# Performance work log

Measured on AMD Instinct MI355X. Metric: run time of the kernel, lower is better.

## Reference

```python
import jax, jax.numpy as jnp
import numpy as np

B, CIN, CNECK, COUT = 8, 128, 128, 256
NV, NF = 10242, 20480  # icosphere level 5: nv = 10*4^5+2, nf = 20*4^5
EPS = 1e-5


def spmatmul(x, rows, cols, vals, m):
    # x: [..., N]; out[..., r] += vals[k] * x[..., cols[k]] for rows[k] == r
    g = x[..., cols] * vals
    return jnp.zeros(x.shape[:-1] + (m,), x.dtype).at[..., rows].add(g)


def conv1x1(x, w, b):
    # x: [B, Cin, N], w: [Cout, Cin], b: [Cout]
    return jnp.einsum('oi,bin->bon', w, x) + b[None, :, None]


def batchnorm1d(x, gamma, beta):
    # training-mode BN over (batch, spatial) per channel, biased variance
    mean = jnp.mean(x, axis=(0, 2), keepdims=True)
    var = jnp.var(x, axis=(0, 2), keepdims=True)
    xhat = (x - mean) * jax.lax.rsqrt(var + EPS)
    return gamma[None, :, None] * xhat + beta[None, :, None]


def setup_inputs() -> dict:
    key = jax.random.key(0)
    ks = jax.random.split(key, 16)

    def coo(k, nrows, per_row, ncols, scale):
        rows = jnp.repeat(jnp.arange(nrows, dtype=jnp.int32), per_row)
        cols = jax.random.randint(k, (nrows * per_row,), 0, ncols, dtype=jnp.int32)
        vals = jax.random.normal(jax.random.fold_in(k, 1), (nrows * per_row,), jnp.float32) * scale
        return rows, cols, vals

    Gr, Gc, Gv = coo(ks[0], 3 * NF, 3, NV, 0.5)
    Lr, Lc, Lv = coo(ks[1], NV, 7, NV, 0.3)
    Fr, Fc, Fv = coo(ks[2], NV, 6, NF, 1.0 / 6.0)

    def nrm(k, shape, scale=1.0):
        return jax.random.normal(k, shape, jnp.float32) * scale

    s_in = 1.0 / np.sqrt(CIN)
    s_nk = 1.0 / np.sqrt(CNECK)
    s_cf = 1.0 / np.sqrt(4 * CNECK)
    return {
        'x': nrm(ks[3], (B, CIN, NV)),
        'w1a': nrm(ks[4], (CNECK, CIN), s_in), 'b1a': nrm(ks[5], (CNECK,), s_in),
        'g1a': jnp.ones((CNECK,), jnp.float32), 'be1a': jnp.zeros((CNECK,), jnp.float32),
        'coeffs': nrm(ks[6], (CNECK * 4, CNECK), s_cf),
        'g2a': jnp.ones((CNECK,), jnp.float32), 'be2a': jnp.zeros((CNECK,), jnp.float32),
        'w3a': nrm(ks[7], (COUT, CNECK), s_nk), 'b3a': nrm(ks[8], (COUT,), s_nk),
        'g3a': jnp.ones((COUT,), jnp.float32), 'be3a': jnp.zeros((COUT,), jnp.float32),
        'w1b': nrm(ks[9], (COUT, CIN), s_in), 'b1b': nrm(ks[10], (COUT,), s_in),
        'g1b': jnp.ones((COUT,), jnp.float32), 'be1b': jnp.zeros((COUT,), jnp.float32),
        'G_vals': Gv, 'L_vals': Lv, 'F2V_vals': Fv,
        'EW': nrm(ks[11], (NF, 3)), 'NS': nrm(ks[12], (NF, 3)),
        'G_rows': Gr, 'G_cols': Gc,
        'L_rows': Lr, 'L_cols': Lc,
        'F2V_rows': Fr, 'F2V_cols': Fc,
    }


def mesh_conv(h, coeffs, G_rows, G_cols, G_vals, L_rows, L_cols, L_vals,
              F2V_rows, F2V_cols, F2V_vals, EW, NS):
    b, c, nv = h.shape
    # gradient on faces: [B,C,3*NF] -> [B,C,3,NF] -> [B,C,NF,3]
    grad_face = spmatmul(h, G_rows, G_cols, G_vals, 3 * NF)
    grad_face = grad_face.reshape(b, c, 3, NF).transpose(0, 1, 3, 2)
    laplacian = spmatmul(h, L_rows, L_cols, L_vals, NV)
    identity = h  # stride=1 => nv_prev == nv
    gf_ew = jnp.sum(grad_face * EW, axis=-1)  # [B,C,NF]
    gf_ns = jnp.sum(grad_face * NS, axis=-1)
    gv_ew = spmatmul(gf_ew, F2V_rows, F2V_cols, F2V_vals, NV)
    gv_ns = spmatmul(gf_ns, F2V_rows, F2V_cols, F2V_vals, NV)
    feat = jnp.stack([identity, laplacian, gv_ew, gv_ns], axis=-1)  # [B,C,NV,4]
    # [B,NV,C*4] @ [C*4,Cout] -> [B,Cout,NV]  (note: no bias added in original forward)
    out = jnp.matmul(feat.transpose(0, 2, 1, 3).reshape(b, nv, c * 4), coeffs)
    return out.transpose(0, 2, 1)


def reference(x, w1a, b1a, g1a, be1a, coeffs, g2a, be2a, w3a, b3a, g3a, be3a,
              w1b, b1b, g1b, be1b, G_vals, L_vals, F2V_vals, EW, NS,
              G_rows, G_cols, L_rows, L_cols, F2V_rows, F2V_cols):
    # shortcut branch: conv_1b -> bn_1b
    x2 = batchnorm1d(conv1x1(x, w1b, b1b), g1b, be1b)
    # main branch
    h = jax.nn.relu(batchnorm1d(conv1x1(x, w1a, b1a), g1a, be1a))
    h = mesh_conv(h, coeffs, G_rows, G_cols, G_vals, L_rows, L_cols, L_vals,
                  F2V_rows, F2V_cols, F2V_vals, EW, NS)
    h = jax.nn.relu(batchnorm1d(h, g2a, be2a))
    x1 = batchnorm1d(conv1x1(h, w3a, b3a), g3a, be3a)
    return jax.nn.relu(x1 + x2)
```

## Files before the change

### kernel.cpp

```cpp
#include <hip/hip_runtime.h>
#include <math.h>

#define BB   8
#define NVV  10242
#define NFF  20480
#define EPSBN 1e-5f
#define GRAM_BLOCKS 1288
#define RSPLIT 16
#define RCHUNK ((GRAM_BLOCKS + RSPLIT - 1) / RSPLIT)

typedef __attribute__((ext_vector_type(8))) short bf16x8_t;
typedef __attribute__((ext_vector_type(4))) float f32x4_t;

__device__ inline float bf2f(ushort u) {
    union { uint i; float f; } v; v.i = ((uint)u) << 16; return v.f;
}
__device__ inline ushort f2bf(float f) {
    union { float f; uint i; } v; v.f = f;
    const uint r = v.i + 0x7fffu + ((v.i >> 16) & 1u);
    return (ushort)(r >> 16);
}
__device__ inline void unpack2(uint w, float& lo, float& hi) {
    union { uint i; float f; } a, b;
    a.i = w << 16; b.i = w & 0xffff0000u;
    lo = a.f; hi = b.f;
}
__device__ inline uint pack2(float lo, float hi) {
    return (uint)f2bf(lo) | ((uint)f2bf(hi) << 16);
}
__device__ inline void fma8(const uint4 hv, const float w, float s[8]) {
    float lo, hi;
    unpack2(hv.x, lo, hi); s[0] = fmaf(w, lo, s[0]); s[1] = fmaf(w, hi, s[1]);
    unpack2(hv.y, lo, hi); s[2] = fmaf(w, lo, s[2]); s[3] = fmaf(w, hi, s[3]);
    unpack2(hv.z, lo, hi); s[4] = fmaf(w, lo, s[4]); s[5] = fmaf(w, hi, s[5]);
    unpack2(hv.w, lo, hi); s[6] = fmaf(w, lo, s[6]); s[7] = fmaf(w, hi, s[7]);
}
__device__ inline void fma8x2(const uint4 hv, const float wa, const float wb,
                              float sa[8], float sb[8]) {
    float lo, hi;
    unpack2(hv.x, lo, hi);
    sa[0] = fmaf(wa, lo, sa[0]); sb[0] = fmaf(wb, lo, sb[0]);
    sa[1] = fmaf(wa, hi, sa[1]); sb[1] = fmaf(wb, hi, sb[1]);
    unpack2(hv.y, lo, hi);
    sa[2] = fmaf(wa, lo, sa[2]); sb[2] = fmaf(wb, lo, sb[2]);
    sa[3] = fmaf(wa, hi, sa[3]); sb[3] = fmaf(wb, hi, sb[3]);
    unpack2(hv.z, lo, hi);
    sa[4] = fmaf(wa, lo, sa[4]); sb[4] = fmaf(wb, lo, sb[4]);
    sa[5] = fmaf(wa, hi, sa[5]); sb[5] = fmaf(wb, hi, sb[5]);
    unpack2(hv.w, lo, hi);
    sa[6] = fmaf(wa, lo, sa[6]); sb[6] = fmaf(wb, lo, sb[6]);
    sa[7] = fmaf(wa, hi, sa[7]); sb[7] = fmaf(wb, hi, sb[7]);
}
__device__ inline uint4 pack8(const float s[8]) {
    uint4 p;
    p.x = pack2(s[0], s[1]); p.y = pack2(s[2], s[3]);
    p.z = pack2(s[4], s[5]); p.w = pack2(s[6], s[7]);
    return p;
}

__global__ __launch_bounds__(256)
void gram_kernel(const float* __restrict__ x, float* __restrict__ gramPart,
                 float* __restrict__ xsumPart, uint* __restrict__ xTu)
{
    __shared__ __align__(16) ushort Ahi[128 * 64];
    __shared__ __align__(16) ushort Alo[128 * 64];
    const int t = threadIdx.x;
    const int l = t & 63, wid = t >> 6;
    const int l15 = l & 15, l4 = l >> 4;
    f32x4_t acc[2][8];
#pragma unroll
    for (int m = 0; m < 2; ++m)
#pragma unroll
        for (int n = 0; n < 8; ++n) acc[m][n] = (f32x4_t){0.f, 0.f, 0.f, 0.f};
    float xs[8] = {0.f, 0.f, 0.f, 0.f, 0.f, 0.f, 0.f, 0.f};

    const int cc = blockIdx.x;
    const int b = cc / 161, tb = cc % 161, v0 = tb * 64;
#pragma unroll
    for (int i = 0; i < 8; ++i) {
        const int item = t + (i << 8);
        const int c = item >> 4, vq = item & 15;
        const int gv = v0 + (vq << 2);
        const float* xp = x + ((size_t)b * 128 + c) * NVV + gv;
        float4 xv = make_float4(0.f, 0.f, 0.f, 0.f);
        if (gv + 4 <= NVV) {
            xv = *reinterpret_cast<const float4*>(xp);
        } else {
            if (gv     < NVV) xv.x = xp[0];
            if (gv + 1 < NVV) xv.y = xp[1];
        }
        xs[i] += xv.x + xv.y + xv.z + xv.w;
        const ushort h0 = f2bf(xv.x), h1 = f2bf(xv.y), h2 = f2bf(xv.z), h3 = f2bf(xv.w);
        const ushort e0 = f2bf(xv.x - bf2f(h0)), e1 = f2bf(xv.y - bf2f(h1));
        const ushort e2 = f2bf(xv.z - bf2f(h2)), e3 = f2bf(xv.w - bf2f(h3));
        uint2 hp, lp;
        hp.x = (uint)h0 | ((uint)h1 << 16); hp.y = (uint)h2 | ((uint)h3 << 16);
        lp.x = (uint)e0 | ((uint)e1 << 16); lp.y = (uint)e2 | ((uint)e3 << 16);
        const int byte = (c << 7) + (vq << 3);
        const int swz = byte ^ ((c & 7) << 4);
        *reinterpret_cast<uint2*>((char*)Ahi + swz) = hp;
        *reinterpret_cast<uint2*>((char*)Alo + swz) = lp;
    }
    __syncthreads();
    {
        const int v = t & 63, cq = t >> 6;
        const int gv = v0 + v;
        if (gv < NVV) {
            uint4* rowp = reinterpret_cast<uint4*>(xTu + ((size_t)b * NVV + gv) * 64) + (cq << 2);
#pragma unroll
            for (int k2 = 0; k2 < 4; ++k2) {
                uint wrd[4];
#pragma unroll
                for (int w2 = 0; w2 < 4; ++w2) {
                    const int c0 = (cq << 5) + (k2 << 3) + (w2 << 1);
                    const int b0 = ((c0) << 7) + (v << 1);
                    const int b1 = ((c0 + 1) << 7) + (v << 1);
                    const ushort q0 = *reinterpret_cast<const ushort*>((const char*)Ahi + (b0 ^ ((c0 & 7) << 4)));
                    const ushort q1 = *reinterpret_cast<const ushort*>((const char*)Ahi + (b1 ^ (((c0 + 1) & 7) << 4)));
                    wrd[w2] = (uint)q0 | ((uint)q1 << 16);
                }
                rowp[k2] = make_uint4(wrd[0], wrd[1], wrd[2], wrd[3]);
            }
        }
    }
#pragma unroll
    for (int kk2 = 0; kk2 < 2; ++kk2) {
        bf16x8_t ah[2], al[2];
#pragma unroll
        for (int m = 0; m < 2; ++m) {
            const int row = wid * 32 + m * 16 + l15;
            const int byte = (row << 7) + (kk2 << 6) + (l4 << 4);
            ah[m] = *reinterpret_cast<const bf16x8_t*>((const char*)Ahi + (byte ^ ((row & 7) << 4)));
            al[m] = *reinterpret_cast<const bf16x8_t*>((const char*)Alo + (byte ^ ((row & 7) << 4)));
        }
#pragma unroll
        for (int n = 0; n < 8; ++n) {
            const int rn = n * 16 + l15;
            const int byte = (rn << 7) + (kk2 << 6) + (l4 << 4);
            const bf16x8_t bh = *reinterpret_cast<const bf16x8_t*>((const char*)Ahi + (byte ^ ((rn & 7) << 4)));
            const bf16x8_t bl = *reinterpret_cast<const bf16x8_t*>((const char*)Alo + (byte ^ ((rn & 7) << 4)));
#pragma unroll
            for (int m = 0; m < 2; ++m) {
                acc[m][n] = __builtin_amdgcn_mfma_f32_16x16x32_bf16(ah[m], bh, acc[m][n], 0, 0, 0);
                acc[m][n] = __builtin_amdgcn_mfma_f32_16x16x32_bf16(ah[m], bl, acc[m][n], 0, 0, 0);
                acc[m][n] = __builtin_amdgcn_mfma_f32_16x16x32_bf16(al[m], bh, acc[m][n], 0, 0, 0);
            }
        }
    }
    float* gp = gramPart + (size_t)blockIdx.x * 16384;
#pragma unroll
    for (int m = 0; m < 2; ++m)
#pragma unroll
        for (int n = 0; n < 8; ++n)
#pragma unroll
            for (int j = 0; j < 4; ++j) {
                const int row = wid * 32 + m * 16 + l4 * 4 + j;
                const int col = n * 16 + l15;
                gp[row * 128 + col] = acc[m][n][j];
            }
#pragma unroll
    for (int i = 0; i < 8; ++i) {
        xs[i] += __shfl_xor(xs[i], 1);
        xs[i] += __shfl_xor(xs[i], 2);
        xs[i] += __shfl_xor(xs[i], 4);
        xs[i] += __shfl_xor(xs[i], 8);
    }
    if ((l & 15) == 0) {
#pragma unroll
        for (int i = 0; i < 8; ++i)
            xsumPart[(size_t)blockIdx.x * 128 + wid * 4 + l4 + i * 16] = xs[i];
    }
}

__global__ __launch_bounds__(256)
void reduce_gram1_kernel(const float* __restrict__ gp, float* __restrict__ part2)
{
    const int e = blockIdx.x * 256 + threadIdx.x;
    const int y = blockIdx.y;
    const int i0 = y * RCHUNK;
    const int i1 = (i0 + RCHUNK < GRAM_BLOCKS) ? (i0 + RCHUNK) : GRAM_BLOCKS;
    float s = 0.f;
    for (int i = i0; i < i1; ++i) s += gp[(size_t)i * 16384 + e];
    part2[(size_t)y * 16384 + e] = s;
}

__global__ __launch_bounds__(256)
void reduce_gram2_kernel(const float* __restrict__ part2, const float* __restrict__ xp,
                         float* __restrict__ Gram, float* __restrict__ xsum)
{
    const int e = blockIdx.x * 256 + threadIdx.x;
    float s = 0.f;
#pragma unroll
    for (int y = 0; y < RSPLIT; ++y) s += part2[(size_t)y * 16384 + e];
    Gram[e] = s;
    if (blockIdx.x == 0 && threadIdx.x < 128) {
        float sx = 0.f;
        for (int i = 0; i < GRAM_BLOCKS; ++i) sx += xp[(size_t)i * 128 + threadIdx.x];
        xsum[threadIdx.x] = sx;
    }
}

__global__ __launch_bounds__(128)
void stats_ab_kernel(const float* __restrict__ Gram, const float* __restrict__ xsum,
                     const float* __restrict__ w1a, const float* __restrict__ g1a,
                     const float* __restrict__ be1a,
                     const float* __restrict__ w1b, const float* __restrict__ g1b,
                     const float* __restrict__ be1b,
                     float* __restrict__ alpha_a, float* __restrict__ beta_a,
                     float* __restrict__ alpha_b, float* __restrict__ beta_b)
{
    const int t = threadIdx.x;
    const int cc = blockIdx.x;
    const float invN = 1.f / (float)(BB * NVV);
    const bool isA = cc < 128;
    const int c = isA ? cc : cc - 128;
    const float* Wrow = isA ? (w1a + (size_t)c * 128) : (w1b + (size_t)c * 128);
    __shared__ float Wr[128];
    __shared__ float red[4];
    Wr[t] = Wrow[t];
    __syncthreads();
    float gi = 0.f;
    const float* Grow = Gram + (size_t)t * 128;
    for (int j = 0; j < 128; ++j) gi = fmaf(Grow[j], Wr[j], gi);
    float pi = Wr[t] * gi * invN;
    float qi = (xsum[t] * invN) * Wr[t];
    for (int off = 32; off > 0; off >>= 1) {
        pi += __shfl_down(pi, off);
        qi += __shfl_down(qi, off);
    }
    const int wid = t >> 6;
    if ((t & 63) == 0) { red[wid] = pi; red[2 + wid] = qi; }
    __syncthreads();
    if (t == 0) {
        const float P = red[0] + red[1], Q = red[2] + red[3];
        const float var = P - Q * Q;
        const float g = isA ? g1a[c] : g1b[c];
        const float be = isA ? be1a[c] : be1b[c];
        const float a = g * rsqrtf(var + EPSBN);
        if (isA) { alpha_a[c] = a; beta_a[c] = be - a * Q; }
        else     { alpha_b[c] = a; beta_b[c] = be - a * Q; }
    }
}

__global__ __launch_bounds__(256)
void prepack_weights_kernel(const float* __restrict__ w1a, const float* __restrict__ w1b,
                            const float* __restrict__ w3a, uint* __restrict__ wpk)
{
    const int j = blockIdx.x * 256 + threadIdx.x;
    const int seg = j >> 12;
    const int slab = seg >> 1, kc = (seg & 1) << 6;
    const int u = j & 4095;
    const int o = u >> 5;
    const int inner = (u << 2) & 127;
    const int inner0 = inner ^ ((o & 7) << 4);
    const int kp = inner0 >> 2;
    const float* W;
    if (slab == 0)      W = w1a;
    else if (slab <= 2) W = w1b + (size_t)(slab - 1) * 128 * 128;
    else                W = w3a + (size_t)(slab - 3) * 128 * 128;
    const float2 wv = *reinterpret_cast<const float2*>(&W[(size_t)o * 128 + kc + 2 * kp]);
    wpk[j] = pack2(wv.x, wv.y);
}

__global__ __launch_bounds__(256)
void prepack_coeffs_kernel(const float* __restrict__ coeffs, uint* __restrict__ cpk)
{
    const int j = blockIdx.x * 256 + threadIdx.x;
    const int chunk = j >> 12, u = j & 4095;
    const int o = u >> 5;
    const int inner = (u << 2) & 127;
    const int inner0 = inner ^ ((o & 7) << 4);
    const int p = inner0 >> 2;
    float v0f, v1f;
    if (chunk < 4) {
        const int q = chunk >> 1, c0 = (chunk & 1) << 6;
        const int row0 = (c0 + 2 * p) * 4 + q;
        v0f = coeffs[(size_t)row0 * 128 + o];
        v1f = coeffs[(size_t)(row0 + 4) * 128 + o];
    } else if (chunk < 6) {
        const int c0 = (chunk - 4) << 6;
        v0f = (o == c0 + 2 * p) ? 1.f : 0.f;
        v1f = (o == c0 + 2 * p + 1) ? 1.f : 0.f;
    } else {
        const int kc = chunk - 6;
        const int kg0 = kc * 64 + 2 * p;
        const int row0 = (kg0 < 128) ? (kg0 * 4 + 2) : ((kg0 - 128) * 4 + 3);
        const int row1 = (kg0 + 1 < 128) ? ((kg0 + 1) * 4 + 2) : ((kg0 + 1 - 128) * 4 + 3);
        v0f = coeffs[(size_t)row0 * 128 + o];
        v1f = coeffs[(size_t)row1 * 128 + o];
    }
    cpk[j] = pack2(v0f, v1f);
}

__global__ __launch_bounds__(256)
void build_meta_kernel(const float* __restrict__ Gv, const int* __restrict__ Gc,
                       const float* __restrict__ EW, const float* __restrict__ NSm,
                       int* __restrict__ colp, float2* __restrict__ wp)
{
    const int i = blockIdx.x * 256 + threadIdx.x;
    if (i >= NFF * 9) return;
    const int f = i / 9, m = i - f * 9;
    const int e = m / 3, jj = m - e * 3;
    const size_t gidx = ((size_t)e * NFF + f) * 3 + jj;
    const float g = Gv[gidx];
    colp[i] = Gc[gidx];
    wp[i] = make_float2(EW[f * 3 + e] * g, NSm[f * 3 + e] * g);
}

template <int MODE>
__global__ __launch_bounds__(256)
void mfma_conv_kernel(const ushort* __restrict__ Asrc, const uint4* __restrict__ wpk,
                      const float* __restrict__ aIn, const float* __restrict__ bIn,
                      const float* __restrict__ aA, const float* __restrict__ bA,
                      const float* __restrict__ aB, const float* __restrict__ bB,
                      ushort* __restrict__ hOut, ushort* __restrict__ x2Out,
                      ushort* __restrict__ x1Out,
                      float* __restrict__ statSum, float* __restrict__ statSsq)
{
    __shared__ __align__(16) ushort As[64 * 128];
    __shared__ __align__(16) ushort Bs[128 * 64];
    float* statS = (float*)Bs;
    float* statQ = (float*)Bs + 512;
    const int t = threadIdx.x;
    const int bid = blockIdx.x;
    const int b = bid & 7, vblk = bid >> 3;
    const int v0 = vblk * 64;
    const int l = t & 63, wid = t >> 6;
    const int l15 = l & 15, l4 = l >> 4;

#pragma unroll
    for (int i = 0; i < 4; ++i) {
        const int item = t + (i << 8);
        const int r = item >> 4, piece = item & 15;
        const int cb = piece * 8;
        const int v = v0 + r;
        uint4 pk = make_uint4(0u, 0u, 0u, 0u);
        if (v < NVV) {
            pk = *reinterpret_cast<const uint4*>(Asrc + ((size_t)b * NVV + v) * 128 + cb);
            if (MODE == 1) {
                float s[8];
                unpack2(pk.x, s[0], s[1]); unpack2(pk.y, s[2], s[3]);
                unpack2(pk.z, s[4], s[5]); unpack2(pk.w, s[6], s[7]);
                const float4 a0 = *reinterpret_cast<const float4*>(&aIn[cb]);
                const float4 a1 = *reinterpret_cast<const float4*>(&aIn[cb + 4]);
                const float4 b0 = *reinterpret_cast<const float4*>(&bIn[cb]);
                const float4 b1 = *reinterpret_cast<const float4*>(&bIn[cb + 4]);
                s[0] = fmaxf(fmaf(a0.x, s[0], b0.x), 0.f);
                s[1] = fmaxf(fmaf(a0.y, s[1], b0.y), 0.f);
                s[2] = fmaxf(fmaf(a0.z, s[2], b0.z), 0.f);
                s[3] = fmaxf(fmaf(a0.w, s[3], b0.w), 0.f);
                s[4] = fmaxf(fmaf(a1.x, s[4], b1.x), 0.f);
                s[5] = fmaxf(fmaf(a1.y, s[5], b1.y), 0.f);
                s[6] = fmaxf(fmaf(a1.z, s[6], b1.z), 0.f);
                s[7] = fmaxf(fmaf(a1.w, s[7], b1.w), 0.f);
                pk = pack8(s);
            }
        }
        const int byte = (r << 8) + (piece << 4);
        *reinterpret_cast<uint4*>((char*)As + (byte ^ ((r & 7) << 4))) = pk;
    }

    const int NZ = (MODE == 0) ? 3 : 2;
    for (int z = 0; z < NZ; ++z) {
        const int slab = (MODE == 0) ? z : (3 + z);
        f32x4_t acc[8];
#pragma unroll
        for (int n = 0; n < 8; ++n) acc[n] = (f32x4_t){0.f, 0.f, 0.f, 0.f};

        for (int kc = 0; kc < 128; kc += 64) {
            const uint4* wseg = wpk + (size_t)(slab * 2 + (kc >> 6)) * 1024;
#pragma unroll
            for (int i = 0; i < 4; ++i)
                reinterpret_cast<uint4*>(Bs)[t + (i << 8)] = wseg[t + (i << 8)];
            __syncthreads();
#pragma unroll
            for (int kk2 = 0; kk2 < 2; ++kk2) {
                const int row = wid * 16 + l15;
                const int abyte = (row << 8) + (kc << 1) + (kk2 << 6) + (l4 << 4);
                const bf16x8_t af = *reinterpret_cast<const bf16x8_t*>(
                    (const char*)As + (abyte ^ ((row & 7) << 4)));
#pragma unroll
                for (int n = 0; n < 8; ++n) {
                    const int o = n * 16 + l15;
                    const int bbyte = (o << 7) + (kk2 << 6) + (l4 << 4);
                    const bf16x8_t bfr = *reinterpret_cast<const bf16x8_t*>(
                        (const char*)Bs + (bbyte ^ ((o & 7) << 4)));
                    acc[n] = __builtin_amdgcn_mfma_f32_16x16x32_bf16(af, bfr, acc[n], 0, 0, 0);
                }
            }
            __syncthreads();
        }

        if (MODE == 0 && z == 0) {
            float aO[8], bO[8];
#pragma unroll
            for (int n = 0; n < 8; ++n) {
                const int c = n * 16 + l15;
                aO[n] = aA[c]; bO[n] = bA[c];
            }
#pragma unroll
            for (int j = 0; j < 4; ++j) {
                const int v = v0 + wid * 16 + l4 * 4 + j;
                if (v < NVV) {
                    ushort* mp = hOut + ((size_t)b * NVV + v) * 128 + l15;
#pragma unroll
                    for (int n = 0; n < 8; ++n)
                        mp[n * 16] = f2bf(fmaxf(fmaf(aO[n], acc[n][j], bO[n]), 0.f));
                }
            }
        } else if (MODE == 0) {
            float aO[8], bO[8];
#pragma unroll
            for (int n = 0; n < 8; ++n) {
                const int cl = n * 16 + l15;
                aO[n] = aB[(z - 1) * 128 + cl]; bO[n] = bB[(z - 1) * 128 + cl];
            }
            const int vbase = v0 + wid * 16 + l4 * 4;
#pragma unroll
            for (int n = 0; n < 8; ++n) {
                const int cl = n * 16 + l15;
                const int ch = (z - 1) * 128 + cl;
                ushort* p = x2Out + ((size_t)b * 256 + ch) * NVV + vbase;
                if (vbase + 4 <= NVV) {
                    uint* pu = (uint*)p;
                    pu[0] = pack2(fmaf(aO[n], acc[n][0], bO[n]),
                                  fmaf(aO[n], acc[n][1], bO[n]));
                    pu[1] = pack2(fmaf(aO[n], acc[n][2], bO[n]),
                                  fmaf(aO[n], acc[n][3], bO[n]));
                } else {
#pragma unroll
                    for (int j = 0; j < 4; ++j)
                        if (vbase + j < NVV)
                            p[j] = f2bf(fmaf(aO[n], acc[n][j], bO[n]));
                }
            }
        } else {
            float ss[8], sq[8];
#pragma unroll
            for (int n = 0; n < 8; ++n) { ss[n] = 0.f; sq[n] = 0.f; }
            const int vbase = v0 + wid * 16 + l4 * 4;
#pragma unroll
            for (int n = 0; n < 8; ++n) {
                const int cl = n * 16 + l15;
                const int ch = z * 128 + cl;
                ushort* p = x1Out + ((size_t)b * 256 + ch) * NVV + vbase;
                if (vbase + 4 <= NVV) {
                    float v0f = acc[n][0], v1f = acc[n][1];
                    float v2f = acc[n][2], v3f = acc[n][3];
                    uint* pu = (uint*)p;
                    pu[0] = pack2(v0f, v1f);
                    pu[1] = pack2(v2f, v3f);
                    ss[n] += v0f + v1f + v2f + v3f;
                    sq[n] = fmaf(v0f, v0f, sq[n]); sq[n] = fmaf(v1f, v1f, sq[n]);
                    sq[n] = fmaf(v2f, v2f, sq[n]); sq[n] = fmaf(v3f, v3f, sq[n]);
                } else {
#pragma unroll
                    for (int j = 0; j < 4; ++j) {
                        if (vbase + j < NVV) {
                            const float val = acc[n][j];
                            p[j] = f2bf(val);
                            ss[n] += val;
                            sq[n] = fmaf(val, val, sq[n]);
                        }
                    }
                }
            }
#pragma unroll
            for (int n = 0; n < 8; ++n) {
                ss[n] += __shfl_xor(ss[n], 16); ss[n] += __shfl_xor(ss[n], 32);
                sq[n] += __shfl_xor(sq[n], 16); sq[n] += __shfl_xor(sq[n], 32);
            }
            __syncthreads();
            if (l < 16) {
#pragma unroll
                for (int n = 0; n < 8; ++n) {
                    statS[wid * 128 + n * 16 + l] = ss[n];
                    statQ[wid * 128 + n * 16 + l] = sq[n];
                }
            }
            __syncthreads();
            if (t < 128) {
                const int slot = b * 161 + vblk;
                statSum[((size_t)z * 1288 + slot) * 128 + t] =
                    statS[t] + statS[128 + t] + statS[256 + t] + statS[384 + t];
                statSsq[((size_t)z * 1288 + slot) * 128 + t] =
                    statQ[t] + statQ[128 + t] + statQ[256 + t] + statQ[384 + t];
            }
            __syncthreads();
        }
    }
}

__global__ __launch_bounds__(256)
void face_gemm_kernel(const ushort* __restrict__ h, const uint4* __restrict__ fBpk,
                      const int* __restrict__ colp, const float2* __restrict__ wp,
                      ushort* __restrict__ gface)
{
    __shared__ __align__(16) ushort Fg[4][64 * 64];
    __shared__ __align__(16) ushort Bs[128 * 64];
    const int t = threadIdx.x;
    const int bid = blockIdx.x;
    const int b = bid & 7;
    const int f0 = (bid >> 3) * 64;
    const int l = t & 63, wid = t >> 6;
    const int l15 = l & 15, l4 = l >> 4;
    const ushort* hb = h + (size_t)b * NVV * 128;

#pragma unroll
    for (int it = 0; it < 4; ++it) {
        const int idx = t + (it << 8);
        const int r = idx >> 4, p = idx & 15;
        const int cb = p * 8;
        const int base = (f0 + r) * 9;
        float se[8] = {0.f, 0.f, 0.f, 0.f, 0.f, 0.f, 0.f, 0.f};
        float sn[8] = {0.f, 0.f, 0.f, 0.f, 0.f, 0.f, 0.f, 0.f};
#pragma unroll
        for (int m = 0; m < 9; ++m) {
            const int col = colp[base + m];
            const float2 w = wp[base + m];
            const uint4 hv = *reinterpret_cast<const uint4*>(hb + (size_t)col * 128 + cb);
            fma8x2(hv, w.x, w.y, se, sn);
        }
        const int ch = cb >> 6;
        const int piece = (cb & 63) >> 3;
        const int byte = (r << 7) + (piece << 4);
        const int swz = byte ^ ((r & 7) << 4);
        *reinterpret_cast<uint4*>((char*)Fg[ch] + swz)     = pack8(se);
        *reinterpret_cast<uint4*>((char*)Fg[2 + ch] + swz) = pack8(sn);
    }
    __syncthreads();

    f32x4_t acc[8];
#pragma unroll
    for (int n = 0; n < 8; ++n) acc[n] = (f32x4_t){0.f, 0.f, 0.f, 0.f};

    for (int chunk = 0; chunk < 4; ++chunk) {
#pragma unroll
        for (int i = 0; i < 4; ++i)
            reinterpret_cast<uint4*>(Bs)[t + (i << 8)] = fBpk[chunk * 1024 + t + (i << 8)];
        __syncthreads();
#pragma unroll
        for (int kk2 = 0; kk2 < 2; ++kk2) {
            const int row = wid * 16 + l15;
            const int abyte = (row << 7) + (kk2 << 6) + (l4 << 4);
            const bf16x8_t af = *reinterpret_cast<const bf16x8_t*>(
                (const char*)Fg[chunk] + (abyte ^ ((row & 7) << 4)));
#pragma unroll
            for (int n = 0; n < 8; ++n) {
                const int o = n * 16 + l15;
                const int bbyte = (o << 7) + (kk2 << 6) + (l4 << 4);
                const bf16x8_t bfr = *reinterpret_cast<const bf16x8_t*>(
                    (const char*)Bs + (bbyte ^ ((o & 7) << 4)));
                acc[n] = __builtin_amdgcn_mfma_f32_16x16x32_bf16(af, bfr, acc[n], 0, 0, 0);
            }
        }
        __syncthreads();
    }

#pragma unroll
    for (int j = 0; j < 4; ++j) {
        const int r = wid * 16 + l4 * 4 + j;
        const int f = f0 + r;
        ushort* gp = gface + ((size_t)b * NFF + f) * 128 + l15;
#pragma unroll
        for (int n = 0; n < 8; ++n)
            gp[n * 16] = f2bf(acc[n][j]);
    }
}

__global__ __launch_bounds__(256)
void mesh_gemm_kernel(const ushort* __restrict__ h, const ushort* __restrict__ gface,
                      const uint4* __restrict__ cpk,
                      const float* __restrict__ Lv, const int* __restrict__ Lc,
                      const float* __restrict__ Fv, const int* __restrict__ Fc,
                      ushort* __restrict__ meshraw,
                      float* __restrict__ msum, float* __restrict__ mssq)
{
    __shared__ __align__(16) ushort As[64 * 64];
    __shared__ __align__(16) ushort Bs[128 * 64];
    float* statS = (float*)Bs;
    float* statQ = (float*)Bs + 512;
    __shared__ int   LciS[448];
    __shared__ float LwS[448];
    __shared__ int   FciS[384];
    __shared__ float FwS[384];
    const int t = threadIdx.x;
    const int bid = blockIdx.x;
    const int b = bid & 7;
    const int vblk = bid >> 3;
    const int v0 = vblk * 64;
    const int l = t & 63, wid = t >> 6;
    const int l15 = l & 15, l4 = l >> 4;
    const size_t hb = (size_t)b * NVV * 128;

    for (int i = t; i < 448; i += 256) {
        const int g = v0 * 7 + i;
        if (g < NVV * 7) { LciS[i] = Lc[g]; LwS[i] = Lv[g]; }
    }
    for (int i = t; i < 384; i += 256) {
        const int g = v0 * 6 + i;
        if (g < NVV * 6) { FciS[i] = Fc[g]; FwS[i] = Fv[g]; }
    }
    __syncthreads();

    f32x4_t acc[8];
#pragma unroll
    for (int n = 0; n < 8; ++n) acc[n] = (f32x4_t){0.f, 0.f, 0.f, 0.f};

    for (int chunk = 0; chunk < 6; ++chunk) {
        const int q = chunk >> 1, c0 = (chunk & 1) << 6;
#pragma unroll
        for (int i = 0; i < 2; ++i) {
            const int item = t + (i << 8);
            const int r = item >> 3, piece = item & 7;
            const int cb = c0 + piece * 8;
            const int v = v0 + r;
            uint4 pk = make_uint4(0u, 0u, 0u, 0u);
            if (v < NVV) {
                if (q == 0) {
                    pk = *reinterpret_cast<const uint4*>(h + hb + (size_t)v * 128 + cb);
                } else if (q == 1) {
                    float s[8] = {0.f, 0.f, 0.f, 0.f, 0.f, 0.f, 0.f, 0.f};
#pragma unroll
                    for (int j = 0; j < 7; ++j) {
                        const float w = LwS[r * 7 + j];
                        const int col = LciS[r * 7 + j];
                        const uint4 hv = *reinterpret_cast<const uint4*>(h + hb + (size_t)col * 128 + cb);
                        fma8(hv, w, s);
                    }
                    pk = pack8(s);
                } else {
                    float s[8] = {0.f, 0.f, 0.f, 0.f, 0.f, 0.f, 0.f, 0.f};
#pragma unroll
                    for (int j = 0; j < 6; ++j) {
                        const float w = FwS[r * 6 + j];
                        const int f = FciS[r * 6 + j];
                        const uint4 gv = *reinterpret_cast<const uint4*>(
                            gface + ((size_t)b * NFF + f) * 128 + cb);
                        fma8(gv, w, s);
                    }
                    pk = pack8(s);
                }
            }
            const int byte = (r << 7) + (piece << 4);
            *reinterpret_cast<uint4*>((char*)As + (byte ^ ((r & 7) << 4))) = pk;
        }
#pragma unroll
        for (int i = 0; i < 4; ++i) {
            const int idx = t + (i << 8);
            reinterpret_cast<uint4*>(Bs)[idx] = cpk[chunk * 1024 + idx];
        }
        __syncthreads();
#pragma unroll
        for (int kk2 = 0; kk2 < 2; ++kk2) {
            const int row = wid * 16 + l15;
            const int abyte = (row << 7) + (kk2 << 6) + (l4 << 4);
            const bf16x8_t af = *reinterpret_cast<const bf16x8_t*>(
                (const char*)As + (abyte ^ ((row & 7) << 4)));
#pragma unroll
            for (int n = 0; n < 8; ++n) {
                const int o = n * 16 + l15;
                const int bbyte = (o << 7) + (kk2 << 6) + (l4 << 4);
                const bf16x8_t bfr = *reinterpret_cast<const bf16x8_t*>(
                    (const char*)Bs + (bbyte ^ ((o & 7) << 4)));
                acc[n] = __builtin_amdgcn_mfma_f32_16x16x32_bf16(af, bfr, acc[n], 0, 0, 0);
            }
        }
        __syncthreads();
    }
    float ss[8], sq[8];
#pragma unroll
    for (int n = 0; n < 8; ++n) { ss[n] = 0.f; sq[n] = 0.f; }
#pragma unroll
    for (int j = 0; j < 4; ++j) {
        const int row = wid * 16 + l4 * 4 + j;
        const int v = v0 + row;
        if (v < NVV) {
            ushort* mp = meshraw + hb + (size_t)v * 128 + l15;
#pragma unroll
            for (int n = 0; n < 8; ++n) {
                const float val = acc[n][j];
                mp[n * 16] = f2bf(val);
                ss[n] += val;
                sq[n] = fmaf(val, val, sq[n]);
            }
        }
    }
#pragma unroll
    for (int n = 0; n < 8; ++n) {
        ss[n] += __shfl_xor(ss[n], 16); ss[n] += __shfl_xor(ss[n], 32);
        sq[n] += __shfl_xor(sq[n], 16); sq[n] += __shfl_xor(sq[n], 32);
    }
    __syncthreads();
    if (l < 16) {
#pragma unroll
        for (int n = 0; n < 8; ++n) {
            statS[wid * 128 + n * 16 + l] = ss[n];
            statQ[wid * 128 + n * 16 + l] = sq[n];
        }
    }
    __syncthreads();
    if (t < 128) {
        const int blk = b * 161 + vblk;
        msum[(size_t)blk * 128 + t] = statS[t] + statS[128 + t] + statS[256 + t] + statS[384 + t];
        mssq[(size_t)blk * 128 + t] = statQ[t] + statQ[128 + t] + statQ[256 + t] + statQ[384 + t];
    }
}

__global__ __launch_bounds__(256)
void finalize_stats_kernel(const float* __restrict__ s, const float* __restrict__ q, int count,
                           const float* __restrict__ g, const float* __restrict__ be,
                           float* __restrict__ alpha, float* __restrict__ beta, int split)
{
    const int c = blockIdx.x, t = threadIdx.x;
    const size_t base = split ? ((size_t)(c >> 7) * count * 128 + (c & 127)) : (size_t)c;
    float ls = 0.f, lq = 0.f;
    for (int i = t; i < count; i += 256) {
        ls += s[base + (size_t)i * 128];
        lq += q[base + (size_t)i * 128];
    }
    __shared__ float rs[256], rq[256];
    rs[t] = ls; rq[t] = lq;
    __syncthreads();
    for (int off = 128; off > 0; off >>= 1) {
        if (t < off) { rs[t] += rs[t + off]; rq[t] += rq[t + off]; }
        __syncthreads();
    }
    if (t == 0) {
        const float invN = 1.f / (float)(BB * NVV);
        const float mean = rs[0] * invN;
        const float var = rq[0] * invN - mean * mean;
        const float a = g[c] * rsqrtf(var + EPSBN);
        alpha[c] = a;
        beta[c] = be[c] - a * mean;
    }
}

__global__ __launch_bounds__(256)
void final_kernel(float* __restrict__ out, const ushort* __restrict__ x1,
                  const ushort* __restrict__ x2,
                  const float* __restrict__ alpha3, const float* __restrict__ beta3)
{
    const int blk = blockIdx.x;
    const int o = blk & 255;
    const float a = alpha3[o], bb = beta3[o];
    float2* po = reinterpret_cast<float2*>(out + (size_t)blk * NVV);
    const uint* p1 = reinterpret_cast<const uint*>(x1 + (size_t)blk * NVV);
    const uint* p2 = reinterpret_cast<const uint*>(x2 + (size_t)blk * NVV);
    for (int i = threadIdx.x; i < NVV / 2; i += 256) {
        float a1, b1, a2, b2;
        unpack2(p1[i], a1, b1);
        unpack2(p2[i], a2, b2);
        po[i] = make_float2(fmaxf(fmaf(a, a1, bb) + a2, 0.f),
                            fmaxf(fmaf(a, b1, bb) + b2, 0.f));
    }
}

extern "C" void kernel_launch(void* const* d_in, const int* in_sizes, int n_in,
                              void* d_out, int out_size, void* d_ws, size_t ws_size,
                              hipStream_t stream)
{
    (void)in_sizes; (void)n_in; (void)out_size;
    const float* x      = (const float*)d_in[0];
    const float* w1a    = (const float*)d_in[1];
    const float* g1a    = (const float*)d_in[3];
    const float* be1a   = (const float*)d_in[4];
    const float* coeffs = (const float*)d_in[5];
    const float* g2a    = (const float*)d_in[6];
    const float* be2a   = (const float*)d_in[7];
    const float* w3a    = (const float*)d_in[8];
    const float* g3a    = (const float*)d_in[10];
    const float* be3a   = (const float*)d_in[11];
    const float* w1b    = (const float*)d_in[12];
    const float* g1b    = (const float*)d_in[14];
    const float* be1b   = (const float*)d_in[15];
    const float* Gv     = (const float*)d_in[16];
    const float* Lv     = (const float*)d_in[17];
    const float* Fv     = (const float*)d_in[18];
    const float* EW     = (const float*)d_in[19];
    const float* NSm    = (const float*)d_in[20];
    const int*   Gc     = (const int*)d_in[22];
    const int*   Lc     = (const int*)d_in[24];
    const int*   Fc     = (const int*)d_in[26];

    char* base = (char*)d_ws;
    size_t off = 0;
    auto alloc = [&](size_t bytes) { char* p = base + off; off += (bytes + 255) & ~(size_t)255; return p; };

    const size_t r0Bytes = (size_t)GRAM_BLOCKS * 16384 * 4 + (size_t)GRAM_BLOCKS * 128 * 4 + 4096;
    char* region0   = alloc(r0Bytes);
    float* gramPart = (float*)region0;
    float* xsumPart = (float*)(region0 + (size_t)GRAM_BLOCKS * 16384 * 4);
    ushort* gface   = (ushort*)region0;
    ushort* x1      = (ushort*)region0;

    ushort* xT      = (ushort*)alloc((size_t)BB * NVV * 128 * 2);
    ushort* h       = (ushort*)alloc((size_t)BB * NVV * 128 * 2);
    ushort* meshraw = (ushort*)alloc((size_t)BB * NVV * 128 * 2);
    ushort* x2      = (ushort*)alloc((size_t)BB * 256 * NVV * 2);
    uint*  cpk      = (uint*)alloc(40960 * 4);
    uint*  wpk      = (uint*)alloc(40960 * 4);
    int*   colp     = (int*)alloc((size_t)NFF * 9 * 4);
    float2* wp      = (float2*)alloc((size_t)NFF * 9 * 8);
    float* part2    = (float*)alloc((size_t)RSPLIT * 16384 * 4);
    float* Gram     = (float*)alloc(16384 * 4);
    float* xsum     = (float*)alloc(128 * 4);
    float* alpha_a  = (float*)alloc(128 * 4);
    float* beta_a   = (float*)alloc(128 * 4);
    float* alpha_b  = (float*)alloc(256 * 4);
    float* beta_b   = (float*)alloc(256 * 4);
    float* alpha2   = (float*)alloc(128 * 4);
    float* beta2    = (float*)alloc(128 * 4);
    float* alpha3   = (float*)alloc(256 * 4);
    float* beta3    = (float*)alloc(256 * 4);
    float* msum     = (float*)alloc((size_t)1288 * 128 * 4);
    float* mssq     = (float*)alloc((size_t)1288 * 128 * 4);
    float* x1sum    = (float*)alloc((size_t)2 * 1288 * 128 * 4);
    float* x1ssq    = (float*)alloc((size_t)2 * 1288 * 128 * 4);
    if (off > ws_size) return;

    gram_kernel<<<GRAM_BLOCKS, 256, 0, stream>>>(x, gramPart, xsumPart, (uint*)xT);
    reduce_gram1_kernel<<<dim3(64, RSPLIT), 256, 0, stream>>>(gramPart, part2);
    reduce_gram2_kernel<<<64, 256, 0, stream>>>(part2, xsumPart, Gram, xsum);
    stats_ab_kernel<<<384, 128, 0, stream>>>(Gram, xsum, w1a, g1a, be1a, w1b, g1b, be1b,
                                             alpha_a, beta_a, alpha_b, beta_b);
    prepack_coeffs_kernel<<<160, 256, 0, stream>>>(coeffs, cpk);
    prepack_weights_kernel<<<160, 256, 0, stream>>>(w1a, w1b, w3a, wpk);
    build_meta_kernel<<<(NFF * 9 + 255) / 256, 256, 0, stream>>>(Gv, Gc, EW, NSm, colp, wp);
    mfma_conv_kernel<0><<<1288, 256, 0, stream>>>(
        xT, (const uint4*)wpk, nullptr, nullptr, alpha_a, beta_a, alpha_b, beta_b,
        h, x2, nullptr, nullptr, nullptr);
    face_gemm_kernel<<<(NFF / 64) * 8, 256, 0, stream>>>(
        h, (const uint4*)cpk + 6 * 1024, colp, wp, gface);
    mesh_gemm_kernel<<<1288, 256, 0, stream>>>(h, gface, (const uint4*)cpk,
                                               Lv, Lc, Fv, Fc, meshraw, msum, mssq);
    finalize_stats_kernel<<<128, 256, 0, stream>>>(msum, mssq, 1288, g2a, be2a, alpha2, beta2, 0);
    mfma_conv_kernel<1><<<1288, 256, 0, stream>>>(
        meshraw, (const uint4*)wpk, alpha2, beta2, nullptr, nullptr, nullptr, nullptr,
        nullptr, nullptr, x1, x1sum, x1ssq);
    finalize_stats_kernel<<<256, 256, 0, stream>>>(x1sum, x1ssq, 1288, g3a, be3a, alpha3, beta3, 1);
    final_kernel<<<2048, 256, 0, stream>>>((float*)d_out, x1, x2, alpha3, beta3);
}
```

Baseline: 295.8 us.

## Store per-block Gram partials as bf16 pairs, vectorize xT transpose writes

The per-block 128x128 Gram partials are now packed into bf16 pairs before being written, which halves the workspace traffic in gram_kernel and in the first reduction pass. The reduction now unpacks the pairs, and its split count drops from 16 to 8. The xT transpose store is restructured so each thread reads 8-byte LDS chunks and writes full 16-byte rows, replacing the many 2-byte LDS reads. Rounding the partials to bf16 before summing 1288 of them lowers the precision of the Gram matrix that feeds the BN statistics.

```diff
diff --git a/kernel.cpp b/kernel.cpp
--- a/kernel.cpp
+++ b/kernel.cpp
@@ -6,7 +6,7 @@
 #define NFF  20480
 #define EPSBN 1e-5f
 #define GRAM_BLOCKS 1288
-#define RSPLIT 16
+#define RSPLIT 8
 #define RCHUNK ((GRAM_BLOCKS + RSPLIT - 1) / RSPLIT)
 
 typedef __attribute__((ext_vector_type(8))) short bf16x8_t;
@@ -59,7 +59,7 @@
 }
 
 __global__ __launch_bounds__(256)
-void gram_kernel(const float* __restrict__ x, float* __restrict__ gramPart,
+void gram_kernel(const float* __restrict__ x, uint* __restrict__ gramPartU,
                  float* __restrict__ xsumPart, uint* __restrict__ xTu)
 {
     __shared__ __align__(16) ushort Ahi[128 * 64];
@@ -103,23 +103,33 @@
     }
     __syncthreads();
     {
-        const int v = t & 63, cq = t >> 6;
-        const int gv = v0 + v;
-        if (gv < NVV) {
-            uint4* rowp = reinterpret_cast<uint4*>(xTu + ((size_t)b * NVV + gv) * 64) + (cq << 2);
-#pragma unroll
-            for (int k2 = 0; k2 < 4; ++k2) {
-                uint wrd[4];
-#pragma unroll
-                for (int w2 = 0; w2 < 4; ++w2) {
-                    const int c0 = (cq << 5) + (k2 << 3) + (w2 << 1);
-                    const int b0 = ((c0) << 7) + (v << 1);
-                    const int b1 = ((c0 + 1) << 7) + (v << 1);
-                    const ushort q0 = *reinterpret_cast<const ushort*>((const char*)Ahi + (b0 ^ ((c0 & 7) << 4)));
-                    const ushort q1 = *reinterpret_cast<const ushort*>((const char*)Ahi + (b1 ^ (((c0 + 1) & 7) << 4)));
-                    wrd[w2] = (uint)q0 | ((uint)q1 << 16);
+        const int v4 = t >> 4, cg = t & 15;
+        const int gv0 = v0 + v4 * 4;
+        uint rx[8], ry[8];
+#pragma unroll
+        for (int ci = 0; ci < 8; ++ci) {
+            const int c = cg * 8 + ci;
+            const int byte = (c << 7) + (v4 << 3);
+            const uint2 rd = *reinterpret_cast<const uint2*>(
+                (const char*)Ahi + (byte ^ ((c & 7) << 4)));
+            rx[ci] = rd.x; ry[ci] = rd.y;
+        }
+#pragma unroll
+        for (int j = 0; j < 4; ++j) {
+            const int gv = gv0 + j;
+            if (gv < NVV) {
+                uint w[8];
+#pragma unroll
+                for (int ci = 0; ci < 8; ++ci) {
+                    const uint src = (j < 2) ? rx[ci] : ry[ci];
+                    w[ci] = (j & 1) ? (src >> 16) : (src & 0xffffu);
                 }
-                rowp[k2] = make_uint4(wrd[0], wrd[1], wrd[2], wrd[3]);
+                uint4 out;
+                out.x = w[0] | (w[1] << 16);
+                out.y = w[2] | (w[3] << 16);
+                out.z = w[4] | (w[5] << 16);
+                out.w = w[6] | (w[7] << 16);
+                *reinterpret_cast<uint4*>(xTu + ((size_t)b * NVV + gv) * 64 + cg * 4) = out;
             }
         }
     }
@@ -147,16 +157,16 @@
             }
         }
     }
-    float* gp = gramPart + (size_t)blockIdx.x * 16384;
+    uint* gpu = gramPartU + (size_t)blockIdx.x * 8192;
 #pragma unroll
     for (int m = 0; m < 2; ++m)
 #pragma unroll
         for (int n = 0; n < 8; ++n)
 #pragma unroll
-            for (int j = 0; j < 4; ++j) {
-                const int row = wid * 32 + m * 16 + l4 * 4 + j;
+            for (int jp = 0; jp < 2; ++jp) {
+                const int rowpair = wid * 16 + m * 8 + l4 * 2 + jp;
                 const int col = n * 16 + l15;
-                gp[row * 128 + col] = acc[m][n][j];
+                gpu[rowpair * 128 + col] = pack2(acc[m][n][2 * jp], acc[m][n][2 * jp + 1]);
             }
 #pragma unroll
     for (int i = 0; i < 8; ++i) {
@@ -173,15 +183,21 @@
 }
 
 __global__ __launch_bounds__(256)
-void reduce_gram1_kernel(const float* __restrict__ gp, float* __restrict__ part2)
-{
-    const int e = blockIdx.x * 256 + threadIdx.x;
+void reduce_gram1_kernel(const uint* __restrict__ gpu, float* __restrict__ part2)
+{
+    const int pe = blockIdx.x * 256 + threadIdx.x;
     const int y = blockIdx.y;
     const int i0 = y * RCHUNK;
     const int i1 = (i0 + RCHUNK < GRAM_BLOCKS) ? (i0 + RCHUNK) : GRAM_BLOCKS;
-    float s = 0.f;
-    for (int i = i0; i < i1; ++i) s += gp[(size_t)i * 16384 + e];
-    part2[(size_t)y * 16384 + e] = s;
+    float s0 = 0.f, s1 = 0.f;
+    for (int i = i0; i < i1; ++i) {
+        float lo, hi;
+        unpack2(gpu[(size_t)i * 8192 + pe], lo, hi);
+        s0 += lo; s1 += hi;
+    }
+    const int rowpair = pe >> 7, col = pe & 127;
+    part2[(size_t)y * 16384 + (2 * rowpair) * 128 + col]     = s0;
+    part2[(size_t)y * 16384 + (2 * rowpair + 1) * 128 + col] = s1;
 }
 
 __global__ __launch_bounds__(256)
@@ -787,10 +803,10 @@
     size_t off = 0;
     auto alloc = [&](size_t bytes) { char* p = base + off; off += (bytes + 255) & ~(size_t)255; return p; };
 
-    const size_t r0Bytes = (size_t)GRAM_BLOCKS * 16384 * 4 + (size_t)GRAM_BLOCKS * 128 * 4 + 4096;
+    const size_t r0Bytes = (size_t)GRAM_BLOCKS * 8192 * 4 + (size_t)GRAM_BLOCKS * 128 * 4 + 4096;
     char* region0   = alloc(r0Bytes);
-    float* gramPart = (float*)region0;
-    float* xsumPart = (float*)(region0 + (size_t)GRAM_BLOCKS * 16384 * 4);
+    uint*  gramPartU = (uint*)region0;
+    float* xsumPart = (float*)(region0 + (size_t)GRAM_BLOCKS * 8192 * 4);
     ushort* gface   = (ushort*)region0;
     ushort* x1      = (ushort*)region0;
 
@@ -819,8 +835,8 @@
     float* x1ssq    = (float*)alloc((size_t)2 * 1288 * 128 * 4);
     if (off > ws_size) return;
 
-    gram_kernel<<<GRAM_BLOCKS, 256, 0, stream>>>(x, gramPart, xsumPart, (uint*)xT);
-    reduce_gram1_kernel<<<dim3(64, RSPLIT), 256, 0, stream>>>(gramPart, part2);
+    gram_kernel<<<GRAM_BLOCKS, 256, 0, stream>>>(x, gramPartU, xsumPart, (uint*)xT);
+    reduce_gram1_kernel<<<dim3(32, RSPLIT), 256, 0, stream>>>(gramPartU, part2);
     reduce_gram2_kernel<<<64, 256, 0, stream>>>(part2, xsumPart, Gram, xsum);
     stats_ab_kernel<<<384, 128, 0, stream>>>(Gram, xsum, w1a, g1a, be1a, w1b, g1b, be1b,
                                              alpha_a, beta_a, alpha_b, beta_b);
```

Result: no change. 297.4 us (+0.5%).
